# Kernel optimization log

Measured on AMD Instinct MI355X. Metric: run time of the kernel, lower is better.

## Reference

```python
import jax, jax.numpy as jnp
import numpy as np


def setup_inputs() -> dict:
    key = jax.random.key(0)
    ks = jax.random.split(key, 8)
    B, N, D = 8, 2048, 128
    s = 1.0 / float(np.sqrt(D))
    node = jax.random.normal(ks[0], (B, N, D), dtype=jnp.float32)
    node_mask = jax.random.randint(ks[1], (B, N), 0, 2, dtype=jnp.int32)
    punctuation_graph = jax.random.randint(ks[2], (B, N, N), 0, 2, dtype=jnp.int32)
    w_nw = jax.random.uniform(ks[3], (1, D), jnp.float32, -s, s)
    b_nw = jax.random.uniform(ks[4], (1,), jnp.float32, -s, s)
    w_self = jax.random.uniform(ks[5], (D, D), jnp.float32, -s, s)
    b_self = jax.random.uniform(ks[6], (D,), jnp.float32, -s, s)
    w_punct = jax.random.uniform(ks[7], (D, D), jnp.float32, -s, s)
    return {"node": node, "node_mask": node_mask, "punctuation_graph": punctuation_graph,
            "w_nw": w_nw, "b_nw": b_nw, "w_self": w_self, "b_self": b_self,
            "w_punct": w_punct, "iteration_steps": 2}


def reference(node, node_mask, punctuation_graph, w_nw, b_nw, w_self, b_self, w_punct, iteration_steps):
    B, N, D = node.shape
    # dd_graph = mask outer product with zeroed diagonal; graph = dd_graph * punctuation_graph
    eye = jnp.eye(N, dtype=punctuation_graph.dtype)
    dd = node_mask[:, None, :] * node_mask[:, :, None] * (1 - eye)[None, :, :]  # [B,N,N]
    graph = dd * punctuation_graph  # [B,N,N] int, binary
    nbr_num = graph.sum(-1)  # [B,N]
    # replace_masked_values(nbr_num, nbr_num>=1, 1): nodes with no neighbors get denom 1
    nbr_f = jnp.where(nbr_num >= 1, nbr_num.astype(node.dtype), jnp.asarray(1.0, node.dtype))
    gmask = graph > 0
    weights = []
    x = node
    for _ in range(iteration_steps):  # small fixed step count
        dw = jax.nn.sigmoid(jnp.einsum('bnd,od->bno', x, w_nw) + b_nw)[..., 0]  # [B,N]
        weights.append(dw)
        self_info = jnp.einsum('bnd,ed->bne', x, w_self) + b_self  # [B,N,D]
        info_p = jnp.einsum('bnd,ed->bne', x, w_punct)  # [B,N,D]
        # node_weight[b,i,j] = dw[b,j] where graph[b,i,j] else 0
        nw = jnp.where(gmask, dw[:, None, :], jnp.asarray(0.0, x.dtype))  # [B,N,N]
        agg = jnp.einsum('bnm,bmd->bnd', nw, info_p) / nbr_f[..., None]
        x = jax.nn.relu(self_info + agg)
    all_weight = jnp.stack(weights, axis=1)  # [B, steps, N]
    return x, all_weight
```

## Files before the change

### kernel.cpp

```cpp
#include <hip/hip_runtime.h>
#include <hip/hip_bf16.h>

#define BB 8
#define NN 2048
#define DD 128

typedef __attribute__((ext_vector_type(8))) __bf16 bf16x8;
typedef __attribute__((ext_vector_type(4))) float f32x4;
typedef __attribute__((ext_vector_type(4))) int   i32x4;

static __device__ __forceinline__ unsigned short f2bf(float f) {
    union { float f; unsigned u; } v; v.f = f;
    unsigned r = (v.u + 0x7FFFu + ((v.u >> 16) & 1u)) >> 16;
    return (unsigned short)r;
}
static __device__ __forceinline__ float bf2f(unsigned short b) {
    union { unsigned u; float f; } v; v.u = ((unsigned)b) << 16;
    return v.f;
}

__global__ __launch_bounds__(256) void kernP3(
    const int* __restrict__ punct, const int* __restrict__ mask,
    const float* __restrict__ w_self, const float* __restrict__ w_punct,
    unsigned* __restrict__ pk, float* __restrict__ scale_g, float* __restrict__ pdm_g,
    unsigned short* __restrict__ wsb, unsigned short* __restrict__ wpb)
{
    const int bid = blockIdx.x;
    const int t = threadIdx.x;

    if (bid >= 2048) {
        const int cb = bid - 2048;
        const float* src = (cb < 8) ? w_self : w_punct;
        unsigned short* dst = (cb < 8) ? wsb : wpb;
        const size_t i0 = (size_t)(cb & 7) * 2048 + (size_t)t * 8;
        f32x4 a = *(const f32x4*)(src + i0);
        f32x4 c = *(const f32x4*)(src + i0 + 4);
        unsigned q0 = f2bf(a.x) | ((unsigned)f2bf(a.y) << 16);
        unsigned q1 = f2bf(a.z) | ((unsigned)f2bf(a.w) << 16);
        unsigned q2 = f2bf(c.x) | ((unsigned)f2bf(c.y) << 16);
        unsigned q3 = f2bf(c.z) | ((unsigned)f2bf(c.w) << 16);
        i32x4 pw = {(int)q0, (int)q1, (int)q2, (int)q3};
        *(i32x4*)(dst + i0) = pw;
        return;
    }

    const int wave = t >> 6, lane = t & 63;
    const int row0 = bid * 8 + wave * 2;
    const int b = row0 >> 11;
    const int* mrow = mask + (size_t)b * NN;

    unsigned mw = 0;
    #pragma unroll
    for (int q = 0; q < 8; ++q) {
        i32x4 m = *(const i32x4*)(mrow + lane * 32 + q * 4);
        unsigned nib = (m.x & 1) | ((m.y & 1) << 1) | ((m.z & 1) << 2) | ((m.w & 1) << 3);
        mw |= nib << (4 * q);
    }

    #pragma unroll
    for (int r = 0; r < 2; ++r) {
        const int row = row0 + r;
        const int i = row & (NN - 1);
        const int mi = mrow[i];
        if (mi == 0) {
            if (lane == 0) { scale_g[row] = 0.f; pdm_g[row] = 0.f; }
            continue;
        }
        const int* prow = punct + (size_t)row * NN;
        i32x4 v[8];
        #pragma unroll
        for (int q = 0; q < 8; ++q)
            v[q] = *(const i32x4*)(prow + lane * 32 + q * 4);
        unsigned wd = 0;
        #pragma unroll
        for (int q = 0; q < 8; ++q) {
            unsigned nib = (v[q].x & 1) | ((v[q].y & 1) << 1)
                         | ((v[q].z & 1) << 2) | ((v[q].w & 1) << 3);
            wd |= nib << (4 * q);
        }
        wd &= mw;
        pk[(size_t)row * 64 + lane] = wd;

        int acc = __popc(wd);
        if ((i >> 5) == lane) acc += (int)((wd >> (i & 31)) & 1u) << 16;
        #pragma unroll
        for (int o = 32; o > 0; o >>= 1) acc += __shfl_xor(acc, o, 64);
        if (lane == 0) {
            const int nall = acc & 0xFFFF;
            const int pd   = acc >> 16;
            const int nbr  = nall - pd;
            scale_g[row] = 1.f / (float)(nbr < 1 ? 1 : nbr);
            pdm_g[row]   = (float)pd;
        }
    }
}

__global__ __launch_bounds__(256) void kernB(
    const float* __restrict__ x,
    const unsigned short* __restrict__ wsb, const unsigned short* __restrict__ wpb,
    const float* __restrict__ w_nw, const float* __restrict__ b_nw,
    const float* __restrict__ b_self,
    const float* __restrict__ scale_g, const float* __restrict__ pdm_g,
    float* __restrict__ si_out, unsigned short* __restrict__ yT_out,
    float* __restrict__ aw_out)
{
    __shared__ unsigned short xt[64*32];
    __shared__ unsigned short wst[128*32];
    __shared__ unsigned short wpt[128*32];
    __shared__ float wnw_l[DD];
    __shared__ float red[256];
    __shared__ float dw_l[64];
    __shared__ float scl_l[64];
    __shared__ float pdm_l[64];
    __shared__ unsigned short ytl[128*72];

    const int n0 = blockIdx.x * 64;
    const int t  = threadIdx.x;
    const int b  = n0 >> 11;
    const int nb = n0 & (NN - 1);

    if (t < DD) wnw_l[t] = w_nw[t];
    if (t >= 128 && t < 192) { scl_l[t-128] = scale_g[n0 + t - 128]; }
    if (t >= 192)            { pdm_l[t-192] = pdm_g[n0 + t - 192]; }
    __syncthreads();

    const int wave = t >> 6, lane = t & 63;
    const int wm = wave >> 1, wn = wave & 1;
    const int quad = lane >> 4, l16 = lane & 15;

    const int n_loc = t >> 2, dq = t & 3;
    const int we = t >> 1,   wh = t & 1;

    f32x4 accs[2][4] = {}; f32x4 accp[2][4] = {};
    float dwpart = 0.f;

    #pragma unroll
    for (int kk = 0; kk < 4; ++kk) {
        const int k0 = kk * 32;
        {
            const float* xs = x + (size_t)(n0 + n_loc) * DD + k0 + dq * 8;
            f32x4 a = *(const f32x4*)xs;
            f32x4 c = *(const f32x4*)(xs + 4);
            const float* wv = &wnw_l[k0 + dq * 8];
            dwpart += a.x*wv[0] + a.y*wv[1] + a.z*wv[2] + a.w*wv[3]
                    + c.x*wv[4] + c.y*wv[5] + c.z*wv[6] + c.w*wv[7];
            unsigned q0 = f2bf(a.x) | ((unsigned)f2bf(a.y) << 16);
            unsigned q1 = f2bf(a.z) | ((unsigned)f2bf(a.w) << 16);
            unsigned q2 = f2bf(c.x) | ((unsigned)f2bf(c.y) << 16);
            unsigned q3 = f2bf(c.z) | ((unsigned)f2bf(c.w) << 16);
            i32x4 pw = {(int)q0,(int)q1,(int)q2,(int)q3};
            *(i32x4*)&xt[n_loc*32 + dq*8] = pw;
        }
        {
            const unsigned short* s1 = wsb + (size_t)we * DD + k0 + wh*16;
            const unsigned short* s2 = wpb + (size_t)we * DD + k0 + wh*16;
            i32x4 a0 = *(const i32x4*)s1;
            i32x4 a1 = *(const i32x4*)(s1 + 8);
            *(i32x4*)&wst[we*32 + wh*16]     = a0;
            *(i32x4*)&wst[we*32 + wh*16 + 8] = a1;
            i32x4 c0 = *(const i32x4*)s2;
            i32x4 c1 = *(const i32x4*)(s2 + 8);
            *(i32x4*)&wpt[we*32 + wh*16]     = c0;
            *(i32x4*)&wpt[we*32 + wh*16 + 8] = c1;
        }
        __syncthreads();
        bf16x8 af[2], bs[4], bp[4];
        #pragma unroll
        for (int mt = 0; mt < 2; ++mt)
            af[mt] = *(const bf16x8*)&xt[(wm*32 + mt*16 + l16)*32 + quad*8];
        #pragma unroll
        for (int nt = 0; nt < 4; ++nt) {
            const int er = wn*64 + nt*16 + l16;
            bs[nt] = *(const bf16x8*)&wst[er*32 + quad*8];
            bp[nt] = *(const bf16x8*)&wpt[er*32 + quad*8];
        }
        #pragma unroll
        for (int mt = 0; mt < 2; ++mt)
            #pragma unroll
            for (int nt = 0; nt < 4; ++nt) {
                accs[mt][nt] = __builtin_amdgcn_mfma_f32_16x16x32_bf16(af[mt], bs[nt], accs[mt][nt], 0, 0, 0);
                accp[mt][nt] = __builtin_amdgcn_mfma_f32_16x16x32_bf16(af[mt], bp[nt], accp[mt][nt], 0, 0, 0);
            }
        __syncthreads();
    }

    red[t] = dwpart;
    __syncthreads();
    if (t < 64) {
        float s = red[4*t] + red[4*t+1] + red[4*t+2] + red[4*t+3] + b_nw[0];
        float dv = 1.f / (1.f + __expf(-s));
        dw_l[t] = dv;
        aw_out[(size_t)b * 2 * NN + nb + t] = dv;
    }
    __syncthreads();

    #pragma unroll
    for (int mt = 0; mt < 2; ++mt) {
        #pragma unroll
        for (int nt = 0; nt < 4; ++nt) {
            const int e = wn*64 + nt*16 + l16;
            const float bsv = b_self[e];
            #pragma unroll
            for (int r = 0; r < 4; ++r) {
                const int nl = wm*32 + mt*16 + quad*4 + r;
                const size_t idx = (size_t)(n0 + nl) * DD + e;
                const float yv = dw_l[nl] * accp[mt][nt][r];
                const unsigned short ub = f2bf(yv);
                const float yvr = bf2f(ub);
                si_out[idx] = accs[mt][nt][r] + bsv - scl_l[nl] * pdm_l[nl] * yvr;
                ytl[e*72 + nl] = ub;
            }
        }
    }
    __syncthreads();
    {
        const int e = t >> 1, half = t & 1;
        const i32x4* src = (const i32x4*)&ytl[e*72 + half*32];
        i32x4 v0 = src[0], v1 = src[1], v2 = src[2], v3 = src[3];
        i32x4* dst = (i32x4*)(yT_out + (size_t)(b*DD + e) * NN + nb + half*32);
        dst[0] = v0; dst[1] = v1; dst[2] = v2; dst[3] = v3;
    }
}

#define OFF_SCL   0u
#define OFF_PDM   256u
#define OFF_WNW   512u
#define OFF_DW    1024u
#define OFF_A     1280u
#define OFF_XT4   1280u
#define OFF_RED   (1280u + 16384u)
#define OFF_B     25856u
#define OFF_WST   25856u
#define OFF_WPT   (25856u + 8192u)
#define OFF_YTL   (25856u + 16384u)
#define SMEM_CB   60672u

__global__ __launch_bounds__(256) void kernCB(
    const unsigned* __restrict__ pk,
    const float* __restrict__ scale_g, const float* __restrict__ pdm_g,
    const unsigned short* __restrict__ yT0,
    float* si,
    const unsigned short* __restrict__ wsb, const unsigned short* __restrict__ wpb,
    const float* __restrict__ w_nw, const float* __restrict__ b_nw,
    const float* __restrict__ b_self,
    unsigned short* __restrict__ yT1,
    float* __restrict__ aw1)
{
    __shared__ char smem[SMEM_CB];
    float*          scl_l = (float*)(smem + OFF_SCL);
    float*          pdm_l = (float*)(smem + OFF_PDM);
    float*          wnw_l = (float*)(smem + OFF_WNW);
    float*          dw_l  = (float*)(smem + OFF_DW);
    unsigned*       pPk   = (unsigned*)(smem + OFF_A);
    unsigned short* xt4   = (unsigned short*)(smem + OFF_XT4);
    float*          red   = (float*)(smem + OFF_RED);
    f32x4*          accL  = (f32x4*)(smem + OFF_B);
    unsigned short* wst   = (unsigned short*)(smem + OFF_WST);
    unsigned short* wpt   = (unsigned short*)(smem + OFF_WPT);
    unsigned short* ytl   = (unsigned short*)(smem + OFF_YTL);

    const int t  = threadIdx.x;
    const int b  = blockIdx.x & 7;
    const int i0 = (blockIdx.x >> 3) * 64;
    const size_t rg0 = (size_t)b * NN + i0;

    #pragma unroll
    for (int r = 0; r < 4; ++r) {
        const int u   = r * 256 + t;
        const int row = u >> 4;
        const int wq  = (u & 15) * 4;
        i32x4 v = *(const i32x4*)(pk + (rg0 + row) * 64 + wq);
        *(i32x4*)&pPk[row * 68 + wq] = v;
    }
    if (t < 64)                   scl_l[t]      = scale_g[rg0 + t];
    else if (t < 128)             pdm_l[t-64]   = pdm_g[rg0 + t - 64];
    else                          wnw_l[t-128]  = w_nw[t-128];
    __syncthreads();

    const int wave = t >> 6, lane = t & 63;
    const int kh = wave >> 1, eh = wave & 1;
    const int quad = lane >> 4, l16 = lane & 15;
    const unsigned short* yTb = yT0 + (size_t)b * DD * NN;

    f32x4 acc[4][4] = {};
    #pragma unroll 4
    for (int ks = 0; ks < 32; ++ks) {
        const int kk = kh * 32 + ks;
        bf16x8 bfr[4];
        #pragma unroll
        for (int nt = 0; nt < 4; ++nt) {
            const int e = eh*64 + nt*16 + l16;
            bfr[nt] = *(const bf16x8*)(yTb + (size_t)e * NN + kk*32 + quad*8);
        }
        bf16x8 af[4];
        #pragma unroll
        for (int mt = 0; mt < 4; ++mt) {
            const unsigned w = pPk[(mt*16 + l16) * 68 + kk];
            const unsigned by = (w >> (quad * 8)) & 0xFFu;
            i32x4 ex;
            ex.x = (int)((((by &   1u) << 7) + ((by &   2u) << 22)) * 0x7Fu);
            ex.y = (int)((((by &   4u) << 5) + ((by &   8u) << 20)) * 0x7Fu);
            ex.z = (int)((((by &  16u) << 3) + ((by &  32u) << 18)) * 0x7Fu);
            ex.w = (int)((((by &  64u) << 1) + ((by & 128u) << 16)) * 0x7Fu);
            union { i32x4 i; bf16x8 h; } cv; cv.i = ex;
            af[mt] = cv.h;
        }
        #pragma unroll
        for (int mt = 0; mt < 4; ++mt)
            #pragma unroll
            for (int nt = 0; nt < 4; ++nt)
                acc[mt][nt] = __builtin_amdgcn_mfma_f32_16x16x32_bf16(af[mt], bfr[nt], acc[mt][nt], 0, 0, 0);
    }

    __syncthreads();
    if (kh == 1) {
        #pragma unroll
        for (int mt = 0; mt < 4; ++mt)
            #pragma unroll
            for (int nt = 0; nt < 4; ++nt)
                accL[(eh*16 + mt*4 + nt)*64 + lane] = acc[mt][nt];
    }
    __syncthreads();

    if (kh == 0) {
        #pragma unroll
        for (int mt = 0; mt < 4; ++mt) {
            float part[4] = {0.f, 0.f, 0.f, 0.f};
            #pragma unroll
            for (int nt = 0; nt < 4; ++nt) {
                f32x4 o = accL[(eh*16 + mt*4 + nt)*64 + lane];
                const int e = eh*64 + nt*16 + l16;
                const float wv = wnw_l[e];
                #pragma unroll
                for (int r = 0; r < 4; ++r) {
                    const int row = mt*16 + quad*4 + r;
                    const size_t idx = (rg0 + row) * DD + e;
                    float xv = si[idx] + scl_l[row] * (acc[mt][nt][r] + o[r]);
                    xv = fmaxf(xv, 0.f);
                    xt4[((e >> 5) * 64 + row) * 32 + (e & 31)] = f2bf(xv);
                    part[r] += xv * wv;
                }
            }
            #pragma unroll
            for (int r = 0; r < 4; ++r) {
                const int row = mt*16 + quad*4 + r;
                red[row * 32 + eh*16 + l16] = part[r];
            }
        }
    }
    __syncthreads();

    if (t < 64) {
        float s = b_nw[0];
        #pragma unroll 8
        for (int c = 0; c < 32; ++c) s += red[t * 32 + c];
        float dv = 1.f / (1.f + __expf(-s));
        dw_l[t] = dv;
        aw1[(size_t)b * 2 * NN + i0 + t] = dv;
    }
    __syncthreads();

    const int wm = kh, wn = eh;
    const int we = t >> 1, wh = t & 1;

    f32x4 accs[2][4] = {}; f32x4 accp[2][4] = {};

    #pragma unroll
    for (int kk = 0; kk < 4; ++kk) {
        const int k0 = kk * 32;
        {
            const unsigned short* s1 = wsb + (size_t)we * DD + k0 + wh*16;
            const unsigned short* s2 = wpb + (size_t)we * DD + k0 + wh*16;
            i32x4 a0 = *(const i32x4*)s1;
            i32x4 a1 = *(const i32x4*)(s1 + 8);
            *(i32x4*)&wst[we*32 + wh*16]     = a0;
            *(i32x4*)&wst[we*32 + wh*16 + 8] = a1;
            i32x4 c0 = *(const i32x4*)s2;
            i32x4 c1 = *(const i32x4*)(s2 + 8);
            *(i32x4*)&wpt[we*32 + wh*16]     = c0;
            *(i32x4*)&wpt[we*32 + wh*16 + 8] = c1;
        }
        __syncthreads();
        bf16x8 af[2], bs[4], bp[4];
        #pragma unroll
        for (int mt = 0; mt < 2; ++mt)
            af[mt] = *(const bf16x8*)&xt4[(kk*64 + wm*32 + mt*16 + l16)*32 + quad*8];
        #pragma unroll
        for (int nt = 0; nt < 4; ++nt) {
            const int er = wn*64 + nt*16 + l16;
            bs[nt] = *(const bf16x8*)&wst[er*32 + quad*8];
            bp[nt] = *(const bf16x8*)&wpt[er*32 + quad*8];
        }
        #pragma unroll
        for (int mt = 0; mt < 2; ++mt)
            #pragma unroll
            for (int nt = 0; nt < 4; ++nt) {
                accs[mt][nt] = __builtin_amdgcn_mfma_f32_16x16x32_bf16(af[mt], bs[nt], accs[mt][nt], 0, 0, 0);
                accp[mt][nt] = __builtin_amdgcn_mfma_f32_16x16x32_bf16(af[mt], bp[nt], accp[mt][nt], 0, 0, 0);
            }
        __syncthreads();
    }

    #pragma unroll
    for (int mt = 0; mt < 2; ++mt) {
        #pragma unroll
        for (int nt = 0; nt < 4; ++nt) {
            const int e = wn*64 + nt*16 + l16;
            const float bsv = b_self[e];
            #pragma unroll
            for (int r = 0; r < 4; ++r) {
                const int nl = wm*32 + mt*16 + quad*4 + r;
                const size_t idx = (rg0 + nl) * DD + e;
                const float yv = dw_l[nl] * accp[mt][nt][r];
                const unsigned short ub = f2bf(yv);
                const float yvr = bf2f(ub);
                si[idx] = accs[mt][nt][r] + bsv - scl_l[nl] * pdm_l[nl] * yvr;
                ytl[e*72 + nl] = ub;
            }
        }
    }
    __syncthreads();
    {
        const int e = t >> 1, half = t & 1;
        const i32x4* src = (const i32x4*)&ytl[e*72 + half*32];
        i32x4 v0 = src[0], v1 = src[1], v2 = src[2], v3 = src[3];
        i32x4* dst = (i32x4*)(yT1 + (size_t)(b*DD + e) * NN + i0 + half*32);
        dst[0] = v0; dst[1] = v1; dst[2] = v2; dst[3] = v3;
    }
}

__global__ __launch_bounds__(256) void kernC4(
    const unsigned* __restrict__ pk,
    const float* __restrict__ scale_g,
    const unsigned short* __restrict__ yT,
    const float* __restrict__ sip,
    float* __restrict__ x_out)
{
    __shared__ unsigned pPk[64 * 68];
    __shared__ float scale_l[64];
    __shared__ f32x4 accL[2][16][64];

    const int t  = threadIdx.x;
    const int b  = blockIdx.x & 7;
    const int i0 = (blockIdx.x >> 3) * 64;
    const size_t rg0 = (size_t)b * NN + i0;

    #pragma unroll
    for (int r = 0; r < 4; ++r) {
        const int u   = r * 256 + t;
        const int row = u >> 4;
        const int wq  = (u & 15) * 4;
        i32x4 v = *(const i32x4*)(pk + (rg0 + row) * 64 + wq);
        *(i32x4*)&pPk[row * 68 + wq] = v;
    }
    if (t < 64) scale_l[t] = scale_g[rg0 + t];
    __syncthreads();

    const int wave = t >> 6, lane = t & 63;
    const int kh = wave >> 1, eh = wave & 1;
    const int quad = lane >> 4, l16 = lane & 15;
    const unsigned short* yTb = yT + (size_t)b * DD * NN;

    f32x4 acc[4][4] = {};

    #pragma unroll 4
    for (int ks = 0; ks < 32; ++ks) {
        const int kk = kh * 32 + ks;
        bf16x8 bfr[4];
        #pragma unroll
        for (int nt = 0; nt < 4; ++nt) {
            const int e = eh*64 + nt*16 + l16;
            bfr[nt] = *(const bf16x8*)(yTb + (size_t)e * NN + kk*32 + quad*8);
        }
        bf16x8 af[4];
        #pragma unroll
        for (int mt = 0; mt < 4; ++mt) {
            const unsigned w = pPk[(mt*16 + l16) * 68 + kk];
            const unsigned by = (w >> (quad * 8)) & 0xFFu;
            i32x4 ex;
            ex.x = (int)((((by &   1u) << 7) + ((by &   2u) << 22)) * 0x7Fu);
            ex.y = (int)((((by &   4u) << 5) + ((by &   8u) << 20)) * 0x7Fu);
            ex.z = (int)((((by &  16u) << 3) + ((by &  32u) << 18)) * 0x7Fu);
            ex.w = (int)((((by &  64u) << 1) + ((by & 128u) << 16)) * 0x7Fu);
            union { i32x4 i; bf16x8 h; } cv; cv.i = ex;
            af[mt] = cv.h;
        }
        #pragma unroll
        for (int mt = 0; mt < 4; ++mt)
            #pragma unroll
            for (int nt = 0; nt < 4; ++nt)
                acc[mt][nt] = __builtin_amdgcn_mfma_f32_16x16x32_bf16(af[mt], bfr[nt], acc[mt][nt], 0, 0, 0);
    }

    __syncthreads();
    if (kh == 1) {
        #pragma unroll
        for (int mt = 0; mt < 4; ++mt)
            #pragma unroll
            for (int nt = 0; nt < 4; ++nt)
                accL[eh][mt*4 + nt][lane] = acc[mt][nt];
    }
    __syncthreads();
    if (kh == 0) {
        #pragma unroll
        for (int mt = 0; mt < 4; ++mt) {
            #pragma unroll
            for (int nt = 0; nt < 4; ++nt) {
                f32x4 o = accL[eh][mt*4 + nt][lane];
                const int e = eh*64 + nt*16 + l16;
                #pragma unroll
                for (int r = 0; r < 4; ++r) {
                    const int row = mt*16 + quad*4 + r;
                    const size_t idx = (rg0 + row) * DD + e;
                    float v = sip[idx] + scale_l[row] * (acc[mt][nt][r] + o[r]);
                    x_out[idx] = fmaxf(v, 0.f);
                }
            }
        }
    }
}

extern "C" void kernel_launch(void* const* d_in, const int* in_sizes, int n_in,
                              void* d_out, int out_size, void* d_ws, size_t ws_size,
                              hipStream_t stream) {
    const float* node   = (const float*)d_in[0];
    const int*   mask   = (const int*)  d_in[1];
    const int*   punct  = (const int*)  d_in[2];
    const float* w_nw   = (const float*)d_in[3];
    const float* b_nw   = (const float*)d_in[4];
    const float* w_self = (const float*)d_in[5];
    const float* b_self = (const float*)d_in[6];
    const float* w_punct= (const float*)d_in[7];

    float* xout = (float*)d_out;
    float* aw   = xout + (size_t)BB * NN * DD;

    char* w = (char*)d_ws;
    float*          si   = (float*)w;
    unsigned short* yT0  = (unsigned short*)(w + (12u << 20));
    unsigned*       pk   = (unsigned*)(w + (16u << 20));
    float*          scl  = (float*)(w + (20u << 20));
    float*          pdm  = (float*)(w + (20u << 20) + (64u << 10));
    unsigned short* wsb  = (unsigned short*)(w + (21u << 20));
    unsigned short* wpb  = (unsigned short*)(w + (21u << 20) + (32u << 10));
    unsigned short* yT1  = (unsigned short*)(w + (24u << 20));

    kernP3<<<dim3(2064), dim3(256), 0, stream>>>(punct, mask, w_self, w_punct,
                                                 pk, scl, pdm, wsb, wpb);
    kernB <<<dim3(256),  dim3(256), 0, stream>>>(node, wsb, wpb, w_nw, b_nw,
                                                 b_self, scl, pdm, si, yT0, aw);
    kernCB<<<dim3(256),  dim3(256), 0, stream>>>(pk, scl, pdm, yT0, si,
                                                 wsb, wpb, w_nw, b_nw, b_self,
                                                 yT1, aw + NN);
    kernC4<<<dim3(256),  dim3(256), 0, stream>>>(pk, scl, yT1, si, xout);
}
```

Baseline: 258.9 us.

## Coalesce punctuation-graph loads and permute bit packing to match

The graph-packing kernel now reads the int32 adjacency rows with lane-contiguous 16-byte loads, making each wavefront load contiguous, instead of giving each lane a private 128-byte strip. Bits are regathered into 32-bit words with ballots, which yields a permuted bit order. The transposed y tiles written by the GEMM kernels are permuted to match. Masked-out rows are no longer skipped early, so every row's graph data is read, and the packed layout must stay consistent with the aggregation kernel.

```diff
diff --git a/kernel.cpp b/kernel.cpp
--- a/kernel.cpp
+++ b/kernel.cpp
@@ -18,8 +18,11 @@
     union { unsigned u; float f; } v; v.u = ((unsigned)b) << 16;
     return v.f;
 }
-
-__global__ __launch_bounds__(256) void kernP3(
+static __device__ __forceinline__ int permk(int nl) {
+    return (nl & 32) | ((nl & 3) << 3) | ((nl & 31) >> 2);
+}
+
+__global__ __launch_bounds__(256) void kernP4(
     const int* __restrict__ punct, const int* __restrict__ mask,
     const float* __restrict__ w_self, const float* __restrict__ w_punct,
     unsigned* __restrict__ pk, float* __restrict__ scale_g, float* __restrict__ pdm_g,
@@ -49,47 +52,52 @@
     const int b = row0 >> 11;
     const int* mrow = mask + (size_t)b * NN;
 
-    unsigned mw = 0;
+    unsigned mn = 0;
     #pragma unroll
     for (int q = 0; q < 8; ++q) {
-        i32x4 m = *(const i32x4*)(mrow + lane * 32 + q * 4);
+        i32x4 m = *(const i32x4*)(mrow + q * 256 + lane * 4);
         unsigned nib = (m.x & 1) | ((m.y & 1) << 1) | ((m.z & 1) << 2) | ((m.w & 1) << 3);
-        mw |= nib << (4 * q);
+        mn |= nib << (4 * q);
     }
 
     #pragma unroll
     for (int r = 0; r < 2; ++r) {
         const int row = row0 + r;
         const int i = row & (NN - 1);
-        const int mi = mrow[i];
-        if (mi == 0) {
-            if (lane == 0) { scale_g[row] = 0.f; pdm_g[row] = 0.f; }
-            continue;
-        }
         const int* prow = punct + (size_t)row * NN;
-        i32x4 v[8];
-        #pragma unroll
-        for (int q = 0; q < 8; ++q)
-            v[q] = *(const i32x4*)(prow + lane * 32 + q * 4);
-        unsigned wd = 0;
+        unsigned* pkrow = pk + (size_t)row * 64;
+
+        int acc = 0;
         #pragma unroll
         for (int q = 0; q < 8; ++q) {
-            unsigned nib = (v[q].x & 1) | ((v[q].y & 1) << 1)
-                         | ((v[q].z & 1) << 2) | ((v[q].w & 1) << 3);
-            wd |= nib << (4 * q);
-        }
-        wd &= mw;
-        pk[(size_t)row * 64 + lane] = wd;
-
-        int acc = __popc(wd);
-        if ((i >> 5) == lane) acc += (int)((wd >> (i & 31)) & 1u) << 16;
+            i32x4 v = *(const i32x4*)(prow + q * 256 + lane * 4);
+            unsigned nib = (v.x & 1) | ((v.y & 1) << 1)
+                         | ((v.z & 1) << 2) | ((v.w & 1) << 3);
+            nib &= (mn >> (4 * q)) & 0xFu;
+            acc += __popc(nib);
+            if (((i >> 8) == q) && (((i >> 2) & 63) == lane))
+                acc += (int)((nib >> (i & 3)) & 1u) << 16;
+            unsigned long long bal0 = __ballot((int)(nib & 1u));
+            unsigned long long bal1 = __ballot((int)(nib & 2u));
+            unsigned long long bal2 = __ballot((int)(nib & 4u));
+            unsigned long long bal3 = __ballot((int)(nib & 8u));
+            if (lane < 8) {
+                const int sh = 8 * lane;
+                unsigned wd =  ((unsigned)(bal0 >> sh) & 0xFFu)
+                            | (((unsigned)(bal1 >> sh) & 0xFFu) << 8)
+                            | (((unsigned)(bal2 >> sh) & 0xFFu) << 16)
+                            | (((unsigned)(bal3 >> sh) & 0xFFu) << 24);
+                pkrow[q * 8 + lane] = wd;
+            }
+        }
         #pragma unroll
         for (int o = 32; o > 0; o >>= 1) acc += __shfl_xor(acc, o, 64);
         if (lane == 0) {
             const int nall = acc & 0xFFFF;
             const int pd   = acc >> 16;
+            const int mi   = mrow[i];
             const int nbr  = nall - pd;
-            scale_g[row] = 1.f / (float)(nbr < 1 ? 1 : nbr);
+            scale_g[row] = mi ? 1.f / (float)(nbr < 1 ? 1 : nbr) : 0.f;
             pdm_g[row]   = (float)pd;
         }
     }
@@ -208,7 +216,7 @@
                 const unsigned short ub = f2bf(yv);
                 const float yvr = bf2f(ub);
                 si_out[idx] = accs[mt][nt][r] + bsv - scl_l[nl] * pdm_l[nl] * yvr;
-                ytl[e*72 + nl] = ub;
+                ytl[e*72 + permk(nl)] = ub;
             }
         }
     }
@@ -415,7 +423,7 @@
                 const unsigned short ub = f2bf(yv);
                 const float yvr = bf2f(ub);
                 si[idx] = accs[mt][nt][r] + bsv - scl_l[nl] * pdm_l[nl] * yvr;
-                ytl[e*72 + nl] = ub;
+                ytl[e*72 + permk(nl)] = ub;
             }
         }
     }
@@ -545,7 +553,7 @@
     unsigned short* wpb  = (unsigned short*)(w + (21u << 20) + (32u << 10));
     unsigned short* yT1  = (unsigned short*)(w + (24u << 20));
 
-    kernP3<<<dim3(2064), dim3(256), 0, stream>>>(punct, mask, w_self, w_punct,
+    kernP4<<<dim3(2064), dim3(256), 0, stream>>>(punct, mask, w_self, w_punct,
                                                  pk, scl, pdm, wsb, wpb);
     kernB <<<dim3(256),  dim3(256), 0, stream>>>(node, wsb, wpb, w_nw, b_nw,
                                                  b_self, scl, pdm, si, yT0, aw);
```

Result: slower. 268.2 us (+3.6%).

## Decouple first-step projection from graph packing and move diagonal correction downstream

Applied to the files above, without the earlier changes.

The first projection kernel now runs before the graph-packing kernel and no longer depends on its row scale and diagonal counts. It converts the fp32 weights to bf16 itself and writes an extra bf16 copy of the dw-scaled punct projection. The diagonal correction is applied later in the second-step kernel instead. This aims to remove the dependency so the two kernels could overlap or run back to back without waiting. It costs an extra 4 MB write plus a later read, and redundant weight conversion in every block; on a single stream the kernels still serialize.

```diff
diff --git a/kernel.cpp b/kernel.cpp
--- a/kernel.cpp
+++ b/kernel.cpp
@@ -19,89 +19,14 @@
     return v.f;
 }
 
-__global__ __launch_bounds__(256) void kernP3(
-    const int* __restrict__ punct, const int* __restrict__ mask,
-    const float* __restrict__ w_self, const float* __restrict__ w_punct,
-    unsigned* __restrict__ pk, float* __restrict__ scale_g, float* __restrict__ pdm_g,
-    unsigned short* __restrict__ wsb, unsigned short* __restrict__ wpb)
-{
-    const int bid = blockIdx.x;
-    const int t = threadIdx.x;
-
-    if (bid >= 2048) {
-        const int cb = bid - 2048;
-        const float* src = (cb < 8) ? w_self : w_punct;
-        unsigned short* dst = (cb < 8) ? wsb : wpb;
-        const size_t i0 = (size_t)(cb & 7) * 2048 + (size_t)t * 8;
-        f32x4 a = *(const f32x4*)(src + i0);
-        f32x4 c = *(const f32x4*)(src + i0 + 4);
-        unsigned q0 = f2bf(a.x) | ((unsigned)f2bf(a.y) << 16);
-        unsigned q1 = f2bf(a.z) | ((unsigned)f2bf(a.w) << 16);
-        unsigned q2 = f2bf(c.x) | ((unsigned)f2bf(c.y) << 16);
-        unsigned q3 = f2bf(c.z) | ((unsigned)f2bf(c.w) << 16);
-        i32x4 pw = {(int)q0, (int)q1, (int)q2, (int)q3};
-        *(i32x4*)(dst + i0) = pw;
-        return;
-    }
-
-    const int wave = t >> 6, lane = t & 63;
-    const int row0 = bid * 8 + wave * 2;
-    const int b = row0 >> 11;
-    const int* mrow = mask + (size_t)b * NN;
-
-    unsigned mw = 0;
-    #pragma unroll
-    for (int q = 0; q < 8; ++q) {
-        i32x4 m = *(const i32x4*)(mrow + lane * 32 + q * 4);
-        unsigned nib = (m.x & 1) | ((m.y & 1) << 1) | ((m.z & 1) << 2) | ((m.w & 1) << 3);
-        mw |= nib << (4 * q);
-    }
-
-    #pragma unroll
-    for (int r = 0; r < 2; ++r) {
-        const int row = row0 + r;
-        const int i = row & (NN - 1);
-        const int mi = mrow[i];
-        if (mi == 0) {
-            if (lane == 0) { scale_g[row] = 0.f; pdm_g[row] = 0.f; }
-            continue;
-        }
-        const int* prow = punct + (size_t)row * NN;
-        i32x4 v[8];
-        #pragma unroll
-        for (int q = 0; q < 8; ++q)
-            v[q] = *(const i32x4*)(prow + lane * 32 + q * 4);
-        unsigned wd = 0;
-        #pragma unroll
-        for (int q = 0; q < 8; ++q) {
-            unsigned nib = (v[q].x & 1) | ((v[q].y & 1) << 1)
-                         | ((v[q].z & 1) << 2) | ((v[q].w & 1) << 3);
-            wd |= nib << (4 * q);
-        }
-        wd &= mw;
-        pk[(size_t)row * 64 + lane] = wd;
-
-        int acc = __popc(wd);
-        if ((i >> 5) == lane) acc += (int)((wd >> (i & 31)) & 1u) << 16;
-        #pragma unroll
-        for (int o = 32; o > 0; o >>= 1) acc += __shfl_xor(acc, o, 64);
-        if (lane == 0) {
-            const int nall = acc & 0xFFFF;
-            const int pd   = acc >> 16;
-            const int nbr  = nall - pd;
-            scale_g[row] = 1.f / (float)(nbr < 1 ? 1 : nbr);
-            pdm_g[row]   = (float)pd;
-        }
-    }
-}
-
-__global__ __launch_bounds__(256) void kernB(
+__global__ __launch_bounds__(256) void kernB0(
     const float* __restrict__ x,
-    const unsigned short* __restrict__ wsb, const unsigned short* __restrict__ wpb,
     const float* __restrict__ w_nw, const float* __restrict__ b_nw,
-    const float* __restrict__ b_self,
-    const float* __restrict__ scale_g, const float* __restrict__ pdm_g,
-    float* __restrict__ si_out, unsigned short* __restrict__ yT_out,
+    const float* __restrict__ w_self, const float* __restrict__ b_self,
+    const float* __restrict__ w_punct,
+    float* __restrict__ si_out,
+    unsigned short* __restrict__ yne_out,
+    unsigned short* __restrict__ yT_out,
     float* __restrict__ aw_out)
 {
     __shared__ unsigned short xt[64*32];
@@ -110,8 +35,6 @@
     __shared__ float wnw_l[DD];
     __shared__ float red[256];
     __shared__ float dw_l[64];
-    __shared__ float scl_l[64];
-    __shared__ float pdm_l[64];
     __shared__ unsigned short ytl[128*72];
 
     const int n0 = blockIdx.x * 64;
@@ -120,8 +43,6 @@
     const int nb = n0 & (NN - 1);
 
     if (t < DD) wnw_l[t] = w_nw[t];
-    if (t >= 128 && t < 192) { scl_l[t-128] = scale_g[n0 + t - 128]; }
-    if (t >= 192)            { pdm_l[t-192] = pdm_g[n0 + t - 192]; }
     __syncthreads();
 
     const int wave = t >> 6, lane = t & 63;
@@ -152,16 +73,36 @@
             *(i32x4*)&xt[n_loc*32 + dq*8] = pw;
         }
         {
-            const unsigned short* s1 = wsb + (size_t)we * DD + k0 + wh*16;
-            const unsigned short* s2 = wpb + (size_t)we * DD + k0 + wh*16;
-            i32x4 a0 = *(const i32x4*)s1;
-            i32x4 a1 = *(const i32x4*)(s1 + 8);
-            *(i32x4*)&wst[we*32 + wh*16]     = a0;
-            *(i32x4*)&wst[we*32 + wh*16 + 8] = a1;
-            i32x4 c0 = *(const i32x4*)s2;
-            i32x4 c1 = *(const i32x4*)(s2 + 8);
-            *(i32x4*)&wpt[we*32 + wh*16]     = c0;
-            *(i32x4*)&wpt[we*32 + wh*16 + 8] = c1;
+            const float* s1 = w_self  + (size_t)we * DD + k0 + wh*16;
+            const float* s2 = w_punct + (size_t)we * DD + k0 + wh*16;
+            f32x4 a0 = *(const f32x4*)s1;      f32x4 a1 = *(const f32x4*)(s1+4);
+            f32x4 a2 = *(const f32x4*)(s1+8);  f32x4 a3 = *(const f32x4*)(s1+12);
+            unsigned q0 = f2bf(a0.x) | ((unsigned)f2bf(a0.y)<<16);
+            unsigned q1 = f2bf(a0.z) | ((unsigned)f2bf(a0.w)<<16);
+            unsigned q2 = f2bf(a1.x) | ((unsigned)f2bf(a1.y)<<16);
+            unsigned q3 = f2bf(a1.z) | ((unsigned)f2bf(a1.w)<<16);
+            unsigned q4 = f2bf(a2.x) | ((unsigned)f2bf(a2.y)<<16);
+            unsigned q5 = f2bf(a2.z) | ((unsigned)f2bf(a2.w)<<16);
+            unsigned q6 = f2bf(a3.x) | ((unsigned)f2bf(a3.y)<<16);
+            unsigned q7 = f2bf(a3.z) | ((unsigned)f2bf(a3.w)<<16);
+            i32x4 pw0 = {(int)q0,(int)q1,(int)q2,(int)q3};
+            i32x4 pw1 = {(int)q4,(int)q5,(int)q6,(int)q7};
+            *(i32x4*)&wst[we*32 + wh*16]     = pw0;
+            *(i32x4*)&wst[we*32 + wh*16 + 8] = pw1;
+            f32x4 c0 = *(const f32x4*)s2;      f32x4 c1 = *(const f32x4*)(s2+4);
+            f32x4 c2 = *(const f32x4*)(s2+8);  f32x4 c3 = *(const f32x4*)(s2+12);
+            unsigned r0 = f2bf(c0.x) | ((unsigned)f2bf(c0.y)<<16);
+            unsigned r1 = f2bf(c0.z) | ((unsigned)f2bf(c0.w)<<16);
+            unsigned r2 = f2bf(c1.x) | ((unsigned)f2bf(c1.y)<<16);
+            unsigned r3 = f2bf(c1.z) | ((unsigned)f2bf(c1.w)<<16);
+            unsigned r4 = f2bf(c2.x) | ((unsigned)f2bf(c2.y)<<16);
+            unsigned r5 = f2bf(c2.z) | ((unsigned)f2bf(c2.w)<<16);
+            unsigned r6 = f2bf(c3.x) | ((unsigned)f2bf(c3.y)<<16);
+            unsigned r7 = f2bf(c3.z) | ((unsigned)f2bf(c3.w)<<16);
+            i32x4 pv0 = {(int)r0,(int)r1,(int)r2,(int)r3};
+            i32x4 pv1 = {(int)r4,(int)r5,(int)r6,(int)r7};
+            *(i32x4*)&wpt[we*32 + wh*16]     = pv0;
+            *(i32x4*)&wpt[we*32 + wh*16 + 8] = pv1;
         }
         __syncthreads();
         bf16x8 af[2], bs[4], bp[4];
@@ -204,10 +145,10 @@
             for (int r = 0; r < 4; ++r) {
                 const int nl = wm*32 + mt*16 + quad*4 + r;
                 const size_t idx = (size_t)(n0 + nl) * DD + e;
+                si_out[idx] = accs[mt][nt][r] + bsv;
                 const float yv = dw_l[nl] * accp[mt][nt][r];
                 const unsigned short ub = f2bf(yv);
-                const float yvr = bf2f(ub);
-                si_out[idx] = accs[mt][nt][r] + bsv - scl_l[nl] * pdm_l[nl] * yvr;
+                yne_out[idx] = ub;
                 ytl[e*72 + nl] = ub;
             }
         }
@@ -219,6 +160,82 @@
         i32x4 v0 = src[0], v1 = src[1], v2 = src[2], v3 = src[3];
         i32x4* dst = (i32x4*)(yT_out + (size_t)(b*DD + e) * NN + nb + half*32);
         dst[0] = v0; dst[1] = v1; dst[2] = v2; dst[3] = v3;
+    }
+}
+
+__global__ __launch_bounds__(256) void kernP3(
+    const int* __restrict__ punct, const int* __restrict__ mask,
+    const float* __restrict__ w_self, const float* __restrict__ w_punct,
+    unsigned* __restrict__ pk, float* __restrict__ scale_g, float* __restrict__ pdm_g,
+    unsigned short* __restrict__ wsb, unsigned short* __restrict__ wpb)
+{
+    const int bid = blockIdx.x;
+    const int t = threadIdx.x;
+
+    if (bid >= 2048) {
+        const int cb = bid - 2048;
+        const float* src = (cb < 8) ? w_self : w_punct;
+        unsigned short* dst = (cb < 8) ? wsb : wpb;
+        const size_t i0 = (size_t)(cb & 7) * 2048 + (size_t)t * 8;
+        f32x4 a = *(const f32x4*)(src + i0);
+        f32x4 c = *(const f32x4*)(src + i0 + 4);
+        unsigned q0 = f2bf(a.x) | ((unsigned)f2bf(a.y) << 16);
+        unsigned q1 = f2bf(a.z) | ((unsigned)f2bf(a.w) << 16);
+        unsigned q2 = f2bf(c.x) | ((unsigned)f2bf(c.y) << 16);
+        unsigned q3 = f2bf(c.z) | ((unsigned)f2bf(c.w) << 16);
+        i32x4 pw = {(int)q0, (int)q1, (int)q2, (int)q3};
+        *(i32x4*)(dst + i0) = pw;
+        return;
+    }
+
+    const int wave = t >> 6, lane = t & 63;
+    const int row0 = bid * 8 + wave * 2;
+    const int b = row0 >> 11;
+    const int* mrow = mask + (size_t)b * NN;
+
+    unsigned mw = 0;
+    #pragma unroll
+    for (int q = 0; q < 8; ++q) {
+        i32x4 m = *(const i32x4*)(mrow + lane * 32 + q * 4);
+        unsigned nib = (m.x & 1) | ((m.y & 1) << 1) | ((m.z & 1) << 2) | ((m.w & 1) << 3);
+        mw |= nib << (4 * q);
+    }
+
+    #pragma unroll
+    for (int r = 0; r < 2; ++r) {
+        const int row = row0 + r;
+        const int i = row & (NN - 1);
+        const int mi = mrow[i];
+        if (mi == 0) {
+            if (lane == 0) { scale_g[row] = 0.f; pdm_g[row] = 0.f; }
+            continue;
+        }
+        const int* prow = punct + (size_t)row * NN;
+        i32x4 v[8];
+        #pragma unroll
+        for (int q = 0; q < 8; ++q)
+            v[q] = *(const i32x4*)(prow + lane * 32 + q * 4);
+        unsigned wd = 0;
+        #pragma unroll
+        for (int q = 0; q < 8; ++q) {
+            unsigned nib = (v[q].x & 1) | ((v[q].y & 1) << 1)
+                         | ((v[q].z & 1) << 2) | ((v[q].w & 1) << 3);
+            wd |= nib << (4 * q);
+        }
+        wd &= mw;
+        pk[(size_t)row * 64 + lane] = wd;
+
+        int acc = __popc(wd);
+        if ((i >> 5) == lane) acc += (int)((wd >> (i & 31)) & 1u) << 16;
+        #pragma unroll
+        for (int o = 32; o > 0; o >>= 1) acc += __shfl_xor(acc, o, 64);
+        if (lane == 0) {
+            const int nall = acc & 0xFFFF;
+            const int pd   = acc >> 16;
+            const int nbr  = nall - pd;
+            scale_g[row] = 1.f / (float)(nbr < 1 ? 1 : nbr);
+            pdm_g[row]   = (float)pd;
+        }
     }
 }
 
@@ -239,6 +256,7 @@
     const unsigned* __restrict__ pk,
     const float* __restrict__ scale_g, const float* __restrict__ pdm_g,
     const unsigned short* __restrict__ yT0,
+    const unsigned short* __restrict__ yne0,
     float* si,
     const unsigned short* __restrict__ wsb, const unsigned short* __restrict__ wpb,
     const float* __restrict__ w_nw, const float* __restrict__ b_nw,
@@ -335,7 +353,9 @@
                 for (int r = 0; r < 4; ++r) {
                     const int row = mt*16 + quad*4 + r;
                     const size_t idx = (rg0 + row) * DD + e;
-                    float xv = si[idx] + scl_l[row] * (acc[mt][nt][r] + o[r]);
+                    const float yv = bf2f(yne0[idx]);
+                    float xv = si[idx]
+                             + scl_l[row] * (acc[mt][nt][r] + o[r] - pdm_l[row] * yv);
                     xv = fmaxf(xv, 0.f);
                     xt4[((e >> 5) * 64 + row) * 32 + (e & 31)] = f2bf(xv);
                     part[r] += xv * wv;
@@ -537,6 +557,7 @@
 
     char* w = (char*)d_ws;
     float*          si   = (float*)w;
+    unsigned short* yne0 = (unsigned short*)(w + (8u  << 20));
     unsigned short* yT0  = (unsigned short*)(w + (12u << 20));
     unsigned*       pk   = (unsigned*)(w + (16u << 20));
     float*          scl  = (float*)(w + (20u << 20));
@@ -545,11 +566,12 @@
     unsigned short* wpb  = (unsigned short*)(w + (21u << 20) + (32u << 10));
     unsigned short* yT1  = (unsigned short*)(w + (24u << 20));
 
+    kernB0<<<dim3(256),  dim3(256), 0, stream>>>(node, w_nw, b_nw, w_self,
+                                                 b_self, w_punct,
+                                                 si, yne0, yT0, aw);
     kernP3<<<dim3(2064), dim3(256), 0, stream>>>(punct, mask, w_self, w_punct,
                                                  pk, scl, pdm, wsb, wpb);
-    kernB <<<dim3(256),  dim3(256), 0, stream>>>(node, wsb, wpb, w_nw, b_nw,
-                                                 b_self, scl, pdm, si, yT0, aw);
-    kernCB<<<dim3(256),  dim3(256), 0, stream>>>(pk, scl, pdm, yT0, si,
+    kernCB<<<dim3(256),  dim3(256), 0, stream>>>(pk, scl, pdm, yT0, yne0, si,
                                                  wsb, wpb, w_nw, b_nw, b_self,
                                                  yT1, aw + NN);
     kernC4<<<dim3(256),  dim3(256), 0, stream>>>(pk, scl, yT1, si, xout);
```

Measured after the change: 263.8 us. No clear change (+1.9%).
